# Kernel optimization log

Hardware: AMD Instinct MI355X
Metric: run time of the kernel (lower is better)

The kernel has to match this reference:

```python
import jax, jax.numpy as jnp
import numpy as np

NUM_EXPERTS = 8
NUM_SLOTS = 4

def setup_inputs() -> dict:
    key = jax.random.key(0)
    k1, k2 = jax.random.split(key)
    B, S, D = 8, 4096, 1024
    x = jax.random.normal(k1, (B, S, D), dtype=jnp.float32)
    W_phi = jax.random.normal(k2, (D, NUM_EXPERTS * NUM_SLOTS), dtype=jnp.float32) * (1.0 / np.sqrt(D))
    b_phi = jnp.zeros((NUM_EXPERTS * NUM_SLOTS,), dtype=jnp.float32)
    return {"x": x, "W_phi": W_phi, "b_phi": b_phi}

def reference(x, W_phi, b_phi):
    B, S, D = x.shape
    E, P = NUM_EXPERTS, NUM_SLOTS
    # phi logits: (B, S, E, P)
    phi_logits = (jnp.einsum('bsd,dk->bsk', x, W_phi) + b_phi).reshape(B, S, E, P)
    # softmax over seq axis (dispatch weights)
    phi_weights = jax.nn.softmax(phi_logits, axis=1)
    # soft slots: weighted sum of tokens per (expert, slot) -> (B, E, P, D)
    # (faithful to expand_dims*multiply*sum-over-seq in the original, fused as einsum)
    soft_slots = jnp.einsum('bsep,bsd->bepd', phi_weights, x)
    expert_inputs = soft_slots.reshape(B, E, P * D)
    expert_weights = jnp.full((B, S, E), 1.0 / E, dtype=x.dtype)
    expert_indices = jnp.broadcast_to(jnp.arange(E, dtype=jnp.int32)[None, None, :], (B, S, E))
    raw_gate_probs = jax.nn.softmax(phi_logits, axis=-1)
    return (expert_weights, expert_indices, phi_weights, soft_slots, expert_inputs, phi_logits, raw_gate_probs)
```

## Files before the change

kernel.cpp:

```cpp
#include <hip/hip_runtime.h>
#include <hip/hip_bf16.h>

#define BB 8
#define SS 4096
#define DD 1024
#define KK 32
#define EE 8
#define PP 4

#define O0 0L
#define O1 262144L
#define O2 524288L
#define O3 1572864L
#define O4 1835008L
#define O5 2097152L
#define O6 3145728L

#define WA 0L
#define WB 8192L
#define WC 16384L
#define WPKH (WC + 2097152L)
#define WPKL (WPKH + 16384L)
#define WEND (WPKL + 16384L)

typedef __attribute__((ext_vector_type(8))) short short8v;
typedef __attribute__((ext_vector_type(4))) float f32x4;

__device__ __forceinline__ unsigned short f2bf(float f) {
    unsigned u = __builtin_bit_cast(unsigned, f);
    unsigned r = (u + 0x7FFFu + ((u >> 16) & 1u)) >> 16;
    return (unsigned short)r;
}
__device__ __forceinline__ float bf2f(unsigned short h) {
    return __builtin_bit_cast(float, (unsigned)h << 16);
}

__global__ __launch_bounds__(256) void k_wprep(const float* __restrict__ Wp,
    unsigned short* __restrict__ wh, unsigned short* __restrict__ wl)
{
    const int t  = blockIdx.x * 256 + threadIdx.x;
    const int l  = t & 63;
    const int tt = (t >> 6) & 1;
    const int ks = t >> 7;
    const int col = tt * 16 + (l & 15);
    const int dbase = ks * 32 + (l >> 4) * 8;
    const long obase = ((long)(ks * 2 + tt) * 64 + l) * 8;
#pragma unroll
    for (int j = 0; j < 8; ++j) {
        const float w = Wp[(long)(dbase + j) * KK + col];
        const unsigned short h = f2bf(w);
        const float lo = w - bf2f(h);
        wh[obase + j] = h;
        wl[obase + j] = f2bf(lo);
    }
}

__global__ __launch_bounds__(256) void k_logits_mfma(const float* __restrict__ x,
    const unsigned short* __restrict__ wh, const unsigned short* __restrict__ wl,
    float* __restrict__ wsP)
{
    const int tid  = threadIdx.x;
    const int wv   = tid >> 6;
    const int lane = tid & 63;
    const int blk  = blockIdx.x;
    const int tile = blk >> 1, half = blk & 1;
    const long tokw = (long)tile * 64 + wv * 16;
    const int mrow = lane & 15;
    const int kg   = lane >> 4;

    const float* xr = x + (tokw + mrow) * DD + half * 512 + kg * 8;
    const uint4* bh = reinterpret_cast<const uint4*>(wh) + (long)half * 16 * 2 * 64 + lane;
    const uint4* bl = reinterpret_cast<const uint4*>(wl) + (long)half * 16 * 2 * 64 + lane;

    f32x4 acc0 = {0.f, 0.f, 0.f, 0.f};
    f32x4 acc1 = {0.f, 0.f, 0.f, 0.f};

#pragma unroll 4
    for (int s = 0; s < 16; ++s) {
        const float4 u0 = *reinterpret_cast<const float4*>(xr + s * 32);
        const float4 u1 = *reinterpret_cast<const float4*>(xr + s * 32 + 4);
        const short8v b0h = __builtin_bit_cast(short8v, bh[(long)(s * 2    ) * 64]);
        const short8v b1h = __builtin_bit_cast(short8v, bh[(long)(s * 2 + 1) * 64]);
        const short8v b0l = __builtin_bit_cast(short8v, bl[(long)(s * 2    ) * 64]);
        const short8v b1l = __builtin_bit_cast(short8v, bl[(long)(s * 2 + 1) * 64]);

        const float xf[8] = {u0.x, u0.y, u0.z, u0.w, u1.x, u1.y, u1.z, u1.w};
        short8v ah, al;
#pragma unroll
        for (int j = 0; j < 8; ++j) {
            const unsigned short h = f2bf(xf[j]);
            ah[j] = (short)h;
            al[j] = (short)f2bf(xf[j] - bf2f(h));
        }
        acc0 = __builtin_amdgcn_mfma_f32_16x16x32_bf16(ah, b0h, acc0, 0, 0, 0);
        acc1 = __builtin_amdgcn_mfma_f32_16x16x32_bf16(ah, b1h, acc1, 0, 0, 0);
        acc0 = __builtin_amdgcn_mfma_f32_16x16x32_bf16(al, b0h, acc0, 0, 0, 0);
        acc1 = __builtin_amdgcn_mfma_f32_16x16x32_bf16(al, b1h, acc1, 0, 0, 0);
        acc0 = __builtin_amdgcn_mfma_f32_16x16x32_bf16(ah, b0l, acc0, 0, 0, 0);
        acc1 = __builtin_amdgcn_mfma_f32_16x16x32_bf16(ah, b1l, acc1, 0, 0, 0);
    }

#pragma unroll
    for (int r = 0; r < 4; ++r) {
        const long tok = tokw + kg * 4 + r;
        float* o = wsP + ((long)half * 32768 + tok) * KK + mrow;
        o[0]  = acc0[r];
        o[16] = acc1[r];
    }
}

__global__ __launch_bounds__(256) void k_comb2(const float* __restrict__ wsP,
    const float* __restrict__ bp, float* __restrict__ out, float* __restrict__ ws)
{
    const int blk = blockIdx.x;
    const int tid = threadIdx.x;
    const int wv  = __builtin_amdgcn_readfirstlane(tid >> 6);
    const long g  = (long)blk * 256 + tid;
    float acc[KK];
#pragma unroll
    for (int k = 0; k < KK; ++k) acc[k] = bp[k];
#pragma unroll
    for (int h = 0; h < 2; ++h) {
        const float4* p = reinterpret_cast<const float4*>(wsP + ((long)h * 32768 + g) * KK);
#pragma unroll
        for (int m = 0; m < 8; ++m) {
            const float4 v = p[m];
            acc[4*m]   += v.x;
            acc[4*m+1] += v.y;
            acc[4*m+2] += v.z;
            acc[4*m+3] += v.w;
        }
    }
    float4* pl = reinterpret_cast<float4*>(out + O5 + g * KK);
#pragma unroll
    for (int m = 0; m < 8; ++m)
        pl[m] = make_float4(acc[4*m], acc[4*m+1], acc[4*m+2], acc[4*m+3]);
    float rg[KK];
#pragma unroll
    for (int e = 0; e < EE; ++e) {
        const float mx = fmaxf(fmaxf(acc[4*e], acc[4*e+1]), fmaxf(acc[4*e+2], acc[4*e+3]));
        float s = 0.f;
#pragma unroll
        for (int p = 0; p < PP; ++p) { rg[4*e+p] = __expf(acc[4*e+p] - mx); s += rg[4*e+p]; }
        const float ri = 1.f / s;
#pragma unroll
        for (int p = 0; p < PP; ++p) rg[4*e+p] *= ri;
    }
    float4* prg = reinterpret_cast<float4*>(out + O6 + g * KK);
#pragma unroll
    for (int m = 0; m < 8; ++m)
        prg[m] = make_float4(rg[4*m], rg[4*m+1], rg[4*m+2], rg[4*m+3]);
    float4* pew = reinterpret_cast<float4*>(out + O0 + g * EE);
    pew[0] = make_float4(0.125f, 0.125f, 0.125f, 0.125f);
    pew[1] = make_float4(0.125f, 0.125f, 0.125f, 0.125f);
    float4* pei = reinterpret_cast<float4*>(out + O1 + g * EE);
    pei[0] = make_float4(0.f, 1.f, 2.f, 3.f);
    pei[1] = make_float4(4.f, 5.f, 6.f, 7.f);

    float m[KK];
#pragma unroll
    for (int k = 0; k < KK; ++k) m[k] = acc[k];
    for (int off = 1; off < 64; off <<= 1) {
#pragma unroll
        for (int k = 0; k < KK; ++k) m[k] = fmaxf(m[k], __shfl_xor(m[k], off));
    }
    __shared__ float lm[4][KK];
    __shared__ float lsum[4][KK];
    if ((tid & 63) == 0) {
#pragma unroll
        for (int k = 0; k < KK; ++k) lm[wv][k] = m[k];
    }
    __syncthreads();
#pragma unroll
    for (int k = 0; k < KK; ++k)
        m[k] = fmaxf(fmaxf(lm[0][k], lm[1][k]), fmaxf(lm[2][k], lm[3][k]));
    float sv[KK];
#pragma unroll
    for (int k = 0; k < KK; ++k) sv[k] = __expf(acc[k] - m[k]);
    for (int off = 1; off < 64; off <<= 1) {
#pragma unroll
        for (int k = 0; k < KK; ++k) sv[k] += __shfl_xor(sv[k], off);
    }
    if ((tid & 63) == 0) {
#pragma unroll
        for (int k = 0; k < KK; ++k) lsum[wv][k] = sv[k];
    }
    __syncthreads();
    if (tid == 0) {
#pragma unroll
        for (int k = 0; k < KK; ++k) {
            ws[WA + (long)blk * 64 + k]      = m[k];
            ws[WA + (long)blk * 64 + 32 + k] = lsum[0][k] + lsum[1][k] + lsum[2][k] + lsum[3][k];
        }
    }
}

__global__ __launch_bounds__(256) void k_logits4(const float* __restrict__ x,
    const float* __restrict__ Wp, const float* __restrict__ bp,
    float* __restrict__ out)
{
    __shared__ float xl[2][64][68];
    __shared__ float wl[2][64][32];
    const int tid  = threadIdx.x;
    const int wv   = __builtin_amdgcn_readfirstlane(tid >> 6);
    const int lane = tid & 63;
    const long tok0 = (long)blockIdx.x * 64;
    const long g   = tok0 + lane;
    const int sr = tid >> 2;
    const int sco = (tid & 3) * 4;
    float acc[8];
#pragma unroll
    for (int j = 0; j < 8; ++j) acc[j] = 0.f;
    float4 xr[4], wr[2];
#pragma unroll
    for (int j = 0; j < 4; ++j)
        xr[j] = *reinterpret_cast<const float4*>(x + (tok0 + sr) * DD + sco + j * 16);
#pragma unroll
    for (int j = 0; j < 2; ++j)
        wr[j] = *reinterpret_cast<const float4*>(Wp + tid * 8 + j * 4);
#pragma unroll
    for (int j = 0; j < 4; ++j)
        *reinterpret_cast<float4*>(&xl[0][sr][sco + j * 16]) = xr[j];
#pragma unroll
    for (int j = 0; j < 2; ++j)
        *reinterpret_cast<float4*>(&wl[0][0][0] + tid * 8 + j * 4) = wr[j];
    __syncthreads();
    for (int c = 0; c < 16; ++c) {
        const int cb = c & 1;
        if (c < 15) {
            const long dg = (long)(c + 1) * 64;
#pragma unroll
            for (int j = 0; j < 4; ++j)
                xr[j] = *reinterpret_cast<const float4*>(
                    x + (tok0 + sr) * DD + dg + sco + j * 16);
#pragma unroll
            for (int j = 0; j < 2; ++j)
                wr[j] = *reinterpret_cast<const float4*>(Wp + dg * KK + tid * 8 + j * 4);
        }
        const float* xb = &xl[cb][lane][0];
        const float* wb = &wl[cb][0][0] + wv * 8;
#pragma unroll 4
        for (int dq = 0; dq < 16; ++dq) {
            const float4 xv = *reinterpret_cast<const float4*>(xb + dq * 4);
#pragma unroll
            for (int dd = 0; dd < 4; ++dd) {
                const float xs = (dd == 0) ? xv.x : (dd == 1) ? xv.y
                               : (dd == 2) ? xv.z : xv.w;
                const float4 w0 = *reinterpret_cast<const float4*>(wb + (dq * 4 + dd) * 32);
                const float4 w1 = *reinterpret_cast<const float4*>(wb + (dq * 4 + dd) * 32 + 4);
                acc[0] = fmaf(xs, w0.x, acc[0]);
                acc[1] = fmaf(xs, w0.y, acc[1]);
                acc[2] = fmaf(xs, w0.z, acc[2]);
                acc[3] = fmaf(xs, w0.w, acc[3]);
                acc[4] = fmaf(xs, w1.x, acc[4]);
                acc[5] = fmaf(xs, w1.y, acc[5]);
                acc[6] = fmaf(xs, w1.z, acc[6]);
                acc[7] = fmaf(xs, w1.w, acc[7]);
            }
        }
        if (c < 15) {
#pragma unroll
            for (int j = 0; j < 4; ++j)
                *reinterpret_cast<float4*>(&xl[cb ^ 1][sr][sco + j * 16]) = xr[j];
#pragma unroll
            for (int j = 0; j < 2; ++j)
                *reinterpret_cast<float4*>(&wl[cb ^ 1][0][0] + tid * 8 + j * 4) = wr[j];
        }
        __syncthreads();
    }
#pragma unroll
    for (int j = 0; j < 8; ++j) acc[j] += bp[wv * 8 + j];
    float* o5 = out + O5 + g * KK + wv * 8;
    *reinterpret_cast<float4*>(o5)     = make_float4(acc[0], acc[1], acc[2], acc[3]);
    *reinterpret_cast<float4*>(o5 + 4) = make_float4(acc[4], acc[5], acc[6], acc[7]);
    float rg[8];
#pragma unroll
    for (int e = 0; e < 2; ++e) {
        const float* aa = &acc[e * 4];
        const float m = fmaxf(fmaxf(aa[0], aa[1]), fmaxf(aa[2], aa[3]));
        float s = 0.f;
#pragma unroll
        for (int p = 0; p < PP; ++p) { rg[e*4+p] = __expf(aa[p] - m); s += rg[e*4+p]; }
        const float ri = 1.f / s;
#pragma unroll
        for (int p = 0; p < PP; ++p) rg[e*4+p] *= ri;
    }
    float* o6 = out + O6 + g * KK + wv * 8;
    *reinterpret_cast<float4*>(o6)     = make_float4(rg[0], rg[1], rg[2], rg[3]);
    *reinterpret_cast<float4*>(o6 + 4) = make_float4(rg[4], rg[5], rg[6], rg[7]);
    if (wv == 0) {
        float4* p = reinterpret_cast<float4*>(out + O0 + g * EE);
        p[0] = make_float4(0.125f, 0.125f, 0.125f, 0.125f);
        p[1] = make_float4(0.125f, 0.125f, 0.125f, 0.125f);
    } else if (wv == 1) {
        float4* p = reinterpret_cast<float4*>(out + O1 + g * EE);
        p[0] = make_float4(0.f, 1.f, 2.f, 3.f);
        p[1] = make_float4(4.f, 5.f, 6.f, 7.f);
    }
}

__global__ __launch_bounds__(256) void k_smpart(const float* __restrict__ out,
                                                float* __restrict__ ws)
{
    const int blk = blockIdx.x;
    const int tid = threadIdx.x;
    const int wv  = __builtin_amdgcn_readfirstlane(tid >> 6);
    const int b = blk >> 4, sc = blk & 15;
    const long s  = (long)sc * 256 + tid;
    const float* row = out + O5 + ((long)b * SS + s) * KK;
    float v[KK];
    const float4* r4 = reinterpret_cast<const float4*>(row);
#pragma unroll
    for (int q = 0; q < 8; ++q) {
        const float4 t = r4[q];
        v[4*q] = t.x; v[4*q+1] = t.y; v[4*q+2] = t.z; v[4*q+3] = t.w;
    }
    float m[KK];
#pragma unroll
    for (int k = 0; k < KK; ++k) m[k] = v[k];
    for (int off = 1; off < 64; off <<= 1) {
#pragma unroll
        for (int k = 0; k < KK; ++k) m[k] = fmaxf(m[k], __shfl_xor(m[k], off));
    }
    __shared__ float lm[4][KK];
    __shared__ float lsum[4][KK];
    if ((tid & 63) == 0) {
#pragma unroll
        for (int k = 0; k < KK; ++k) lm[wv][k] = m[k];
    }
    __syncthreads();
#pragma unroll
    for (int k = 0; k < KK; ++k)
        m[k] = fmaxf(fmaxf(lm[0][k], lm[1][k]), fmaxf(lm[2][k], lm[3][k]));
    float sv[KK];
#pragma unroll
    for (int k = 0; k < KK; ++k) sv[k] = __expf(v[k] - m[k]);
    for (int off = 1; off < 64; off <<= 1) {
#pragma unroll
        for (int k = 0; k < KK; ++k) sv[k] += __shfl_xor(sv[k], off);
    }
    if ((tid & 63) == 0) {
#pragma unroll
        for (int k = 0; k < KK; ++k) lsum[wv][k] = sv[k];
    }
    __syncthreads();
    if (tid == 0) {
#pragma unroll
        for (int k = 0; k < KK; ++k) {
            ws[WA + (long)blk * 64 + k]      = m[k];
            ws[WA + (long)blk * 64 + 32 + k] = lsum[0][k] + lsum[1][k] + lsum[2][k] + lsum[3][k];
        }
    }
}

__global__ __launch_bounds__(256) void k_smcomb(float* __restrict__ ws)
{
    const int tid = threadIdx.x;
    const int b = tid >> 5, k = tid & 31;
    float m = -1e30f, s = 0.f;
    for (int c = 0; c < 16; ++c) {
        const float mc = ws[WA + (long)(b * 16 + c) * 64 + k];
        const float sc = ws[WA + (long)(b * 16 + c) * 64 + 32 + k];
        const float nm = fmaxf(m, mc);
        s = s * __expf(m - nm) + sc * __expf(mc - nm);
        m = nm;
    }
    ws[WB + (long)b * 64 + k]      = m;
    ws[WB + (long)b * 64 + 32 + k] = 1.f / s;
}

__global__ __launch_bounds__(256) void k_pw(float* __restrict__ out,
                                            const float* __restrict__ ws)
{
    const long i4 = (long)blockIdx.x * 256 + threadIdx.x;
    const float4 l4 = reinterpret_cast<const float4*>(out + O5)[i4];
    const long idx = i4 * 4;
    const int b  = (int)(idx >> 17);
    const int k0 = (int)(idx & 31);
    const float* mb = ws + WB + (long)b * 64;
    const float lv[4] = {l4.x, l4.y, l4.z, l4.w};
    float r[4];
#pragma unroll
    for (int j = 0; j < 4; ++j) {
        const int k = k0 + j;
        r[j] = __expf(lv[j] - mb[k]) * mb[32 + k];
    }
    reinterpret_cast<float4*>(out + O2)[i4] = make_float4(r[0], r[1], r[2], r[3]);
}

__global__ __launch_bounds__(256) void k_slots2(const float* __restrict__ x,
    const float* __restrict__ out, float* __restrict__ dst, int SC, int SLEN)
{
    __shared__ float pwl[2][64 * KK];
    const int tid = threadIdx.x;
    const int blk = blockIdx.x;
    const int sc  = blk % SC;
    const int t2  = blk / SC;
    const int dc  = t2 & 3;
    const int b   = t2 >> 2;
    const int d   = dc * 256 + tid;
    float acc[KK];
#pragma unroll
    for (int k = 0; k < KK; ++k) acc[k] = 0.f;
    const long s0 = (long)sc * SLEN;
    const float* pw = out + O2 + ((long)b * SS + s0) * KK;
    const float* xp = x + ((long)b * SS + s0) * DD + d;
    const int NCH = SLEN >> 6;

    float4 r0 = *reinterpret_cast<const float4*>(pw + tid * 8);
    float4 r1 = *reinterpret_cast<const float4*>(pw + tid * 8 + 4);
    *reinterpret_cast<float4*>(&pwl[0][tid * 8])     = r0;
    *reinterpret_cast<float4*>(&pwl[0][tid * 8 + 4]) = r1;
    __syncthreads();

    for (int ch = 0; ch < NCH; ++ch) {
        const int cb = ch & 1;
        if (ch + 1 < NCH) {
            const float* pn = pw + (long)(ch + 1) * 64 * KK;
            r0 = *reinterpret_cast<const float4*>(pn + tid * 8);
            r1 = *reinterpret_cast<const float4*>(pn + tid * 8 + 4);
        }
        const float* xc = xp + (long)ch * 64 * DD;
        const float* pb = &pwl[cb][0];
#pragma unroll 8
        for (int i = 0; i < 64; ++i) {
            const float xv = xc[(long)i * DD];
#pragma unroll
            for (int q = 0; q < 8; ++q) {
                const float4 w = *reinterpret_cast<const float4*>(pb + i * KK + q * 4);
                acc[4*q]   = fmaf(w.x, xv, acc[4*q]);
                acc[4*q+1] = fmaf(w.y, xv, acc[4*q+1]);
                acc[4*q+2] = fmaf(w.z, xv, acc[4*q+2]);
                acc[4*q+3] = fmaf(w.w, xv, acc[4*q+3]);
            }
        }
        if (ch + 1 < NCH) {
            *reinterpret_cast<float4*>(&pwl[cb ^ 1][tid * 8])     = r0;
            *reinterpret_cast<float4*>(&pwl[cb ^ 1][tid * 8 + 4]) = r1;
        }
        __syncthreads();
    }
    float* o = dst + ((long)(sc * BB + b) * KK) * DD + d;
#pragma unroll
    for (int k = 0; k < KK; ++k) o[(long)k * DD] = acc[k];
}

__global__ __launch_bounds__(256) void k_red(const float* __restrict__ src,
                                             float* __restrict__ out, int SC)
{
    const long i4 = (long)blockIdx.x * 256 + threadIdx.x;
    float4 s = make_float4(0.f, 0.f, 0.f, 0.f);
    const float4* p = reinterpret_cast<const float4*>(src);
    for (int c = 0; c < SC; ++c) {
        const float4 t = p[(long)c * 65536 + i4];
        s.x += t.x; s.y += t.y; s.z += t.z; s.w += t.w;
    }
    reinterpret_cast<float4*>(out + O3)[i4] = s;
    reinterpret_cast<float4*>(out + O4)[i4] = s;
}

extern "C" void kernel_launch(void* const* d_in, const int* in_sizes, int n_in,
                              void* d_out, int out_size, void* d_ws, size_t ws_size,
                              hipStream_t stream)
{
    const float* x  = (const float*)d_in[0];
    const float* Wp = (const float*)d_in[1];
    const float* bp = (const float*)d_in[2];
    float* out = (float*)d_out;
    float* ws  = (float*)d_ws;

    const size_t wfloats = ws_size / 4;

    if (wfloats >= (size_t)WEND) {
        unsigned short* wh = (unsigned short*)(ws + WPKH);
        unsigned short* wl = (unsigned short*)(ws + WPKL);
        hipLaunchKernelGGL(k_wprep,       dim3(16),   dim3(256), 0, stream, Wp, wh, wl);
        hipLaunchKernelGGL(k_logits_mfma, dim3(1024), dim3(256), 0, stream, x, wh, wl, ws + WC);
        hipLaunchKernelGGL(k_comb2,       dim3(128),  dim3(256), 0, stream, ws + WC, bp, out, ws);
    } else {
        hipLaunchKernelGGL(k_logits4, dim3(512), dim3(256), 0, stream, x, Wp, bp, out);
        hipLaunchKernelGGL(k_smpart,  dim3(128), dim3(256), 0, stream, out, ws);
    }

    hipLaunchKernelGGL(k_smcomb, dim3(1),    dim3(256), 0, stream, ws);
    hipLaunchKernelGGL(k_pw,     dim3(1024), dim3(256), 0, stream, out, ws);

    int SC = 0;
    if      (wfloats >= (size_t)(WC + 32L * 262144)) SC = 32;
    else if (wfloats >= (size_t)(WC + 16L * 262144)) SC = 16;
    else if (wfloats >= (size_t)(WC +  8L * 262144)) SC = 8;
    else if (wfloats >= (size_t)(WC +  4L * 262144)) SC = 4;
    else if (wfloats >= (size_t)(WC +  2L * 262144)) SC = 2;
    else if (wfloats >= (size_t)(WC +  1L * 262144)) SC = 1;

    if (SC >= 1) {
        hipLaunchKernelGGL(k_slots2, dim3(BB * 4 * SC), dim3(256), 0, stream,
                           x, out, ws + WC, SC, SS / SC);
        hipLaunchKernelGGL(k_red,    dim3(256), dim3(256), 0, stream, ws + WC, out, SC);
    } else {
        hipLaunchKernelGGL(k_slots2, dim3(BB * 4), dim3(256), 0, stream,
                           x, out, out + O3, 1, SS);
        hipLaunchKernelGGL(k_red,    dim3(256), dim3(256), 0, stream, out + O3, out, 1);
    }
}
```

Baseline: 107.6 us.

## Fuse softmax combine into weight kernel, widen slot accumulation, truncate bf16 split

The single-block softmax-combine kernel is merged into the dispatch-weight kernel, so each block recomputes its batch's max and sum in shared memory and one launch is removed. The slot-accumulation kernel now has each thread handle two adjacent D columns with float2 loads and stores. This halves the block count and doubles the accumulator registers per thread, but reuses each shared-memory weight read twice. The bf16 hi/lo split in the logits MFMA kernel uses bit truncation instead of round-to-nearest conversion, which costs fewer instructions but makes the split error slightly larger.

```diff
diff --git a/kernel.cpp b/kernel.cpp
--- a/kernel.cpp
+++ b/kernel.cpp
@@ -88,9 +88,11 @@
         short8v ah, al;
 #pragma unroll
         for (int j = 0; j < 8; ++j) {
-            const unsigned short h = f2bf(xf[j]);
-            ah[j] = (short)h;
-            al[j] = (short)f2bf(xf[j] - bf2f(h));
+            const unsigned u = __builtin_bit_cast(unsigned, xf[j]);
+            ah[j] = (short)(u >> 16);
+            const float hi = __builtin_bit_cast(float, u & 0xFFFF0000u);
+            const float lo = xf[j] - hi;
+            al[j] = (short)(__builtin_bit_cast(unsigned, lo) >> 16);
         }
         acc0 = __builtin_amdgcn_mfma_f32_16x16x32_bf16(ah, b0h, acc0, 0, 0, 0);
         acc1 = __builtin_amdgcn_mfma_f32_16x16x32_bf16(ah, b1h, acc1, 0, 0, 0);
@@ -353,42 +355,37 @@
     }
 }
 
-__global__ __launch_bounds__(256) void k_smcomb(float* __restrict__ ws)
-{
+__global__ __launch_bounds__(256) void k_pw2(float* __restrict__ out,
+                                             const float* __restrict__ ws)
+{
+    __shared__ float sm[KK], srv[KK];
     const int tid = threadIdx.x;
-    const int b = tid >> 5, k = tid & 31;
-    float m = -1e30f, s = 0.f;
-    for (int c = 0; c < 16; ++c) {
-        const float mc = ws[WA + (long)(b * 16 + c) * 64 + k];
-        const float sc = ws[WA + (long)(b * 16 + c) * 64 + 32 + k];
-        const float nm = fmaxf(m, mc);
-        s = s * __expf(m - nm) + sc * __expf(mc - nm);
-        m = nm;
-    }
-    ws[WB + (long)b * 64 + k]      = m;
-    ws[WB + (long)b * 64 + 32 + k] = 1.f / s;
-}
-
-__global__ __launch_bounds__(256) void k_pw(float* __restrict__ out,
-                                            const float* __restrict__ ws)
-{
-    const long i4 = (long)blockIdx.x * 256 + threadIdx.x;
+    const long i4 = (long)blockIdx.x * 256 + tid;
+    const long idx = i4 * 4;
+    const int b = (int)(idx >> 17);
+    if (tid < KK) {
+        float m = -1e30f, s = 0.f;
+        for (int c = 0; c < 16; ++c) {
+            const float mc = ws[WA + (long)(b * 16 + c) * 64 + tid];
+            const float sc = ws[WA + (long)(b * 16 + c) * 64 + 32 + tid];
+            const float nm = fmaxf(m, mc);
+            s = s * __expf(m - nm) + sc * __expf(mc - nm);
+            m = nm;
+        }
+        sm[tid]  = m;
+        srv[tid] = 1.f / s;
+    }
+    __syncthreads();
     const float4 l4 = reinterpret_cast<const float4*>(out + O5)[i4];
-    const long idx = i4 * 4;
-    const int b  = (int)(idx >> 17);
     const int k0 = (int)(idx & 31);
-    const float* mb = ws + WB + (long)b * 64;
-    const float lv[4] = {l4.x, l4.y, l4.z, l4.w};
-    float r[4];
-#pragma unroll
-    for (int j = 0; j < 4; ++j) {
-        const int k = k0 + j;
-        r[j] = __expf(lv[j] - mb[k]) * mb[32 + k];
-    }
-    reinterpret_cast<float4*>(out + O2)[i4] = make_float4(r[0], r[1], r[2], r[3]);
-}
-
-__global__ __launch_bounds__(256) void k_slots2(const float* __restrict__ x,
+    const float r0 = __expf(l4.x - sm[k0])     * srv[k0];
+    const float r1 = __expf(l4.y - sm[k0 + 1]) * srv[k0 + 1];
+    const float r2 = __expf(l4.z - sm[k0 + 2]) * srv[k0 + 2];
+    const float r3 = __expf(l4.w - sm[k0 + 3]) * srv[k0 + 3];
+    reinterpret_cast<float4*>(out + O2)[i4] = make_float4(r0, r1, r2, r3);
+}
+
+__global__ __launch_bounds__(256) void k_slots4(const float* __restrict__ x,
     const float* __restrict__ out, float* __restrict__ dst, int SC, int SLEN)
 {
     __shared__ float pwl[2][64 * KK];
@@ -396,12 +393,12 @@
     const int blk = blockIdx.x;
     const int sc  = blk % SC;
     const int t2  = blk / SC;
-    const int dc  = t2 & 3;
-    const int b   = t2 >> 2;
-    const int d   = dc * 256 + tid;
-    float acc[KK];
-#pragma unroll
-    for (int k = 0; k < KK; ++k) acc[k] = 0.f;
+    const int dc  = t2 & 1;
+    const int b   = t2 >> 1;
+    const int d   = dc * 512 + tid * 2;
+    float2 acc[KK];
+#pragma unroll
+    for (int k = 0; k < KK; ++k) acc[k] = make_float2(0.f, 0.f);
     const long s0 = (long)sc * SLEN;
     const float* pw = out + O2 + ((long)b * SS + s0) * KK;
     const float* xp = x + ((long)b * SS + s0) * DD + d;
@@ -422,16 +419,20 @@
         }
         const float* xc = xp + (long)ch * 64 * DD;
         const float* pb = &pwl[cb][0];
-#pragma unroll 8
+#pragma unroll 4
         for (int i = 0; i < 64; ++i) {
-            const float xv = xc[(long)i * DD];
+            const float2 xv = *reinterpret_cast<const float2*>(xc + (long)i * DD);
 #pragma unroll
             for (int q = 0; q < 8; ++q) {
                 const float4 w = *reinterpret_cast<const float4*>(pb + i * KK + q * 4);
-                acc[4*q]   = fmaf(w.x, xv, acc[4*q]);
-                acc[4*q+1] = fmaf(w.y, xv, acc[4*q+1]);
-                acc[4*q+2] = fmaf(w.z, xv, acc[4*q+2]);
-                acc[4*q+3] = fmaf(w.w, xv, acc[4*q+3]);
+                acc[4*q].x   = fmaf(w.x, xv.x, acc[4*q].x);
+                acc[4*q].y   = fmaf(w.x, xv.y, acc[4*q].y);
+                acc[4*q+1].x = fmaf(w.y, xv.x, acc[4*q+1].x);
+                acc[4*q+1].y = fmaf(w.y, xv.y, acc[4*q+1].y);
+                acc[4*q+2].x = fmaf(w.z, xv.x, acc[4*q+2].x);
+                acc[4*q+2].y = fmaf(w.z, xv.y, acc[4*q+2].y);
+                acc[4*q+3].x = fmaf(w.w, xv.x, acc[4*q+3].x);
+                acc[4*q+3].y = fmaf(w.w, xv.y, acc[4*q+3].y);
             }
         }
         if (ch + 1 < NCH) {
@@ -442,7 +443,8 @@
     }
     float* o = dst + ((long)(sc * BB + b) * KK) * DD + d;
 #pragma unroll
-    for (int k = 0; k < KK; ++k) o[(long)k * DD] = acc[k];
+    for (int k = 0; k < KK; ++k)
+        *reinterpret_cast<float2*>(o + (long)k * DD) = acc[k];
 }
 
 __global__ __launch_bounds__(256) void k_red(const float* __restrict__ src,
@@ -482,8 +484,7 @@
         hipLaunchKernelGGL(k_smpart,  dim3(128), dim3(256), 0, stream, out, ws);
     }
 
-    hipLaunchKernelGGL(k_smcomb, dim3(1),    dim3(256), 0, stream, ws);
-    hipLaunchKernelGGL(k_pw,     dim3(1024), dim3(256), 0, stream, out, ws);
+    hipLaunchKernelGGL(k_pw2, dim3(1024), dim3(256), 0, stream, out, ws);
 
     int SC = 0;
     if      (wfloats >= (size_t)(WC + 32L * 262144)) SC = 32;
@@ -494,11 +495,11 @@
     else if (wfloats >= (size_t)(WC +  1L * 262144)) SC = 1;
 
     if (SC >= 1) {
-        hipLaunchKernelGGL(k_slots2, dim3(BB * 4 * SC), dim3(256), 0, stream,
+        hipLaunchKernelGGL(k_slots4, dim3(BB * 2 * SC), dim3(256), 0, stream,
                            x, out, ws + WC, SC, SS / SC);
         hipLaunchKernelGGL(k_red,    dim3(256), dim3(256), 0, stream, ws + WC, out, SC);
     } else {
-        hipLaunchKernelGGL(k_slots2, dim3(BB * 4), dim3(256), 0, stream,
+        hipLaunchKernelGGL(k_slots4, dim3(BB * 2), dim3(256), 0, stream,
                            x, out, out + O3, 1, SS);
         hipLaunchKernelGGL(k_red,    dim3(256), dim3(256), 0, stream, out + O3, out, 1);
     }
```

New measurement: 108.7 us. No clear change (+1.0%).
